# Kernel optimization log

Hardware: AMD Instinct MI355X
Metric: run time of the kernel (lower is better)

Reference implementation:

```python
import jax, jax.numpy as jnp
import numpy as np

L, T, DIN, DOUT = 64, 8192, 128, 128

def setup_inputs() -> dict:
    key = jax.random.key(0)
    k1, k2, k3 = jax.random.split(key, 3)
    x = jax.random.normal(k1, (L, T, DIN), dtype=jnp.float32)
    w = jax.random.normal(k2, (L, DIN, DOUT), dtype=jnp.float32)
    b = jax.random.normal(k3, (L, 1, DOUT), dtype=jnp.float32)
    return {"x": x, "w": w, "b": b}

def reference(x, w, b):
    # grouped GEMM: per-layer matmul x[l] @ w[l], fused bias add
    out = jnp.einsum('lti,lio->lto', x, w) + b  # [L, T, DOUT]
    return out
```

## Files before the change

### kernel.cpp

```cpp
#include <hip/hip_runtime.h>
#include <hip/hip_bf16.h>

#define L_N 64
#define T_N 8192
#define K_N 128
#define N_N 128
#define BM  128

typedef __attribute__((ext_vector_type(8))) short short8;
typedef __attribute__((ext_vector_type(4))) float f32x4;

__device__ __forceinline__ unsigned short f2bf(float f) {
    union { float f; unsigned u; } c; c.f = f;
    return (unsigned short)((c.u + 0x7fffu + ((c.u >> 16) & 1u)) >> 16);
}

__global__ __launch_bounds__(256) void wT_kernel(const float* __restrict__ w,
                                                 unsigned short* __restrict__ wT) {
    __shared__ float lds[128 * 129];
    const int l = blockIdx.x;
    const float* wl = w + (size_t)l * (K_N * N_N);
    const int tid = threadIdx.x;
    #pragma unroll 4
    for (int i = 0; i < 64; ++i) {
        int idx = i * 256 + tid;
        int k = idx >> 7, n = idx & 127;
        lds[k * 129 + n] = wl[idx];
    }
    __syncthreads();
    unsigned short* o = wT + (size_t)l * (K_N * N_N);
    #pragma unroll 4
    for (int i = 0; i < 64; ++i) {
        int idx = i * 256 + tid;
        int n = idx >> 7, k = idx & 127;
        o[idx] = f2bf(lds[k * 129 + n]);
    }
}

__global__ __launch_bounds__(256) void gl_kernel(const float* __restrict__ x,
                                                 const unsigned short* __restrict__ wT,
                                                 const float* __restrict__ bias,
                                                 float* __restrict__ out) {
    __shared__ unsigned short xs [BM  * K_N];
    __shared__ unsigned short wsh[N_N * K_N];

    const int tid = threadIdx.x;
    const int l  = blockIdx.x >> 6;
    const int t0 = (blockIdx.x & 63) * BM;
    const float* xg = x + ((size_t)l * T_N + t0) * K_N;

    #pragma unroll
    for (int i = 0; i < 16; ++i) {
        int f = i * 256 + tid;
        const float4 v = ((const float4*)xg)[f];
        int row = f >> 5;
        int kc  = (f & 31) * 4;
        union { unsigned short s[4]; unsigned long long u; } p;
        p.s[0] = f2bf(v.x); p.s[1] = f2bf(v.y); p.s[2] = f2bf(v.z); p.s[3] = f2bf(v.w);
        int us = (row * K_N + kc) ^ ((row & 7) << 3);
        *(unsigned long long*)&xs[us] = p.u;
    }
    const unsigned short* wg = wT + (size_t)l * (K_N * N_N);
    #pragma unroll
    for (int i = 0; i < 8; ++i) {
        int c = i * 256 + tid;
        short8 v = ((const short8*)wg)[c];
        int row = c >> 4;
        int us = (c * 8) ^ ((row & 7) << 3);
        *(short8*)&wsh[us] = v;
    }
    __syncthreads();

    const int wid  = tid >> 6;
    const int lane = tid & 63;
    const int wm = wid >> 1, wn = wid & 1;
    const int lr = lane & 15;
    const int lg = lane >> 4;

    f32x4 acc[4][4];
    #pragma unroll
    for (int mi = 0; mi < 4; ++mi)
        #pragma unroll
        for (int ni = 0; ni < 4; ++ni)
            acc[mi][ni] = (f32x4){0.f, 0.f, 0.f, 0.f};

    #pragma unroll
    for (int kk = 0; kk < 4; ++kk) {
        const int kbase = kk * 32 + lg * 8;
        short8 a[4], bq[4];
        #pragma unroll
        for (int mi = 0; mi < 4; ++mi) {
            int row = wm * 64 + mi * 16 + lr;
            a[mi] = *(const short8*)&xs[(row * K_N + kbase) ^ ((row & 7) << 3)];
        }
        #pragma unroll
        for (int ni = 0; ni < 4; ++ni) {
            int row = wn * 64 + ni * 16 + lr;
            bq[ni] = *(const short8*)&wsh[(row * K_N + kbase) ^ ((row & 7) << 3)];
        }
        #pragma unroll
        for (int mi = 0; mi < 4; ++mi)
            #pragma unroll
            for (int ni = 0; ni < 4; ++ni)
                acc[mi][ni] = __builtin_amdgcn_mfma_f32_16x16x32_bf16(
                                  a[mi], bq[ni], acc[mi][ni], 0, 0, 0);
    }

    float bv[4];
    #pragma unroll
    for (int ni = 0; ni < 4; ++ni)
        bv[ni] = bias[l * N_N + wn * 64 + ni * 16 + lr];

    float* og = out + ((size_t)l * T_N + t0) * N_N;
    #pragma unroll
    for (int mi = 0; mi < 4; ++mi) {
        #pragma unroll
        for (int ni = 0; ni < 4; ++ni) {
            const int col   = wn * 64 + ni * 16 + lr;
            const int rbase = wm * 64 + mi * 16 + lg * 4;
            #pragma unroll
            for (int j = 0; j < 4; ++j)
                og[(size_t)(rbase + j) * N_N + col] = acc[mi][ni][j] + bv[ni];
        }
    }
}

extern "C" void kernel_launch(void* const* d_in, const int* in_sizes, int n_in,
                              void* d_out, int out_size, void* d_ws, size_t ws_size,
                              hipStream_t stream) {
    const float* x = (const float*)d_in[0];
    const float* w = (const float*)d_in[1];
    const float* b = (const float*)d_in[2];
    float* out = (float*)d_out;
    unsigned short* wT = (unsigned short*)d_ws;

    wT_kernel<<<L_N, 256, 0, stream>>>(w, wT);
    gl_kernel<<<L_N * (T_N / BM), 256, 0, stream>>>(x, wT, b, out);
}
```

Baseline: 116.6 us.

## Drop LDS staging; load MFMA fragments directly from global with pre-fragmented weights

The weight prep kernel now writes bf16 weights already laid out in MFMA fragment order, so each lane loads its B operand straight from global memory. The GEMM kernel drops shared memory and __syncthreads entirely: each wave owns a 32-row strip, loads x fragments directly from global, converts them to bf16 in registers, and swaps the operand roles so accumulators map to contiguous output columns, which allows float4 stores. It also adds an XCD-aware block index swizzle and a launch-bounds occupancy hint. The aim is to remove LDS round-trips and barriers and to vectorize stores, at the cost of redundant weight reads across waves and less coalesced x loads.

Result: slower. 142.2 us (+21.9%).

```diff
diff --git a/kernel.cpp b/kernel.cpp
--- a/kernel.cpp
+++ b/kernel.cpp
@@ -5,7 +5,6 @@
 #define T_N 8192
 #define K_N 128
 #define N_N 128
-#define BM  128
 
 typedef __attribute__((ext_vector_type(8))) short short8;
 typedef __attribute__((ext_vector_type(4))) float f32x4;
@@ -15,112 +14,107 @@
     return (unsigned short)((c.u + 0x7fffu + ((c.u >> 16) & 1u)) >> 16);
 }
 
-__global__ __launch_bounds__(256) void wT_kernel(const float* __restrict__ w,
-                                                 unsigned short* __restrict__ wT) {
-    __shared__ float lds[128 * 129];
+__global__ __launch_bounds__(256) void wfrag_kernel(const float* __restrict__ w,
+                                                    unsigned short* __restrict__ wf) {
+    __shared__ float lds[K_N * 129];
     const int l = blockIdx.x;
     const float* wl = w + (size_t)l * (K_N * N_N);
     const int tid = threadIdx.x;
-    #pragma unroll 4
-    for (int i = 0; i < 64; ++i) {
-        int idx = i * 256 + tid;
-        int k = idx >> 7, n = idx & 127;
-        lds[k * 129 + n] = wl[idx];
+    #pragma unroll
+    for (int i = 0; i < 16; ++i) {
+        int f = i * 256 + tid;
+        float4 v = ((const float4*)wl)[f];
+        int k = f >> 5, n = (f & 31) * 4;
+        lds[k * 129 + n + 0] = v.x;
+        lds[k * 129 + n + 1] = v.y;
+        lds[k * 129 + n + 2] = v.z;
+        lds[k * 129 + n + 3] = v.w;
     }
     __syncthreads();
-    unsigned short* o = wT + (size_t)l * (K_N * N_N);
-    #pragma unroll 4
-    for (int i = 0; i < 64; ++i) {
-        int idx = i * 256 + tid;
-        int n = idx >> 7, k = idx & 127;
-        o[idx] = f2bf(lds[k * 129 + n]);
+    unsigned short* o = wf + (size_t)l * (N_N * K_N);
+    #pragma unroll
+    for (int c = 0; c < 16; ++c) {
+        int chunk = c * 256 + tid;
+        int j0   = (chunk & 1) * 4;
+        int lane = (chunk >> 1) & 63;
+        int kk   = (chunk >> 7) & 3;
+        int ni   = chunk >> 9;
+        int n  = ni * 16 + (lane & 15);
+        int kb = kk * 32 + (lane >> 4) * 8 + j0;
+        ushort4 ov;
+        ov.x = f2bf(lds[(kb + 0) * 129 + n]);
+        ov.y = f2bf(lds[(kb + 1) * 129 + n]);
+        ov.z = f2bf(lds[(kb + 2) * 129 + n]);
+        ov.w = f2bf(lds[(kb + 3) * 129 + n]);
+        ((ushort4*)o)[chunk] = ov;
     }
 }
 
-__global__ __launch_bounds__(256) void gl_kernel(const float* __restrict__ x,
-                                                 const unsigned short* __restrict__ wT,
-                                                 const float* __restrict__ bias,
-                                                 float* __restrict__ out) {
-    __shared__ unsigned short xs [BM  * K_N];
-    __shared__ unsigned short wsh[N_N * K_N];
+__global__ __launch_bounds__(256, 3) void gl_kernel(const float* __restrict__ x,
+                                                    const unsigned short* __restrict__ wf,
+                                                    const float* __restrict__ bias,
+                                                    float* __restrict__ out) {
+    const int tid  = threadIdx.x;
+    const int lane = tid & 63;
+    const int wid  = tid >> 6;
+    const int lr   = lane & 15;
+    const int lg   = lane >> 4;
 
-    const int tid = threadIdx.x;
-    const int l  = blockIdx.x >> 6;
-    const int t0 = (blockIdx.x & 63) * BM;
-    const float* xg = x + ((size_t)l * T_N + t0) * K_N;
+    const int bid = blockIdx.x;
+    const int swz = (bid & 7) * 512 + (bid >> 3);
+    const int l    = swz >> 6;
+    const int tile = swz & 63;
+    const int strip = tile * 128 + wid * 32;
 
+    const float* xg = x + ((size_t)l * T_N + strip) * K_N;
+    const unsigned short* wl = wf + (size_t)l * (N_N * K_N);
+
+    f32x4 acc[2][8];
     #pragma unroll
-    for (int i = 0; i < 16; ++i) {
-        int f = i * 256 + tid;
-        const float4 v = ((const float4*)xg)[f];
-        int row = f >> 5;
-        int kc  = (f & 31) * 4;
-        union { unsigned short s[4]; unsigned long long u; } p;
-        p.s[0] = f2bf(v.x); p.s[1] = f2bf(v.y); p.s[2] = f2bf(v.z); p.s[3] = f2bf(v.w);
-        int us = (row * K_N + kc) ^ ((row & 7) << 3);
-        *(unsigned long long*)&xs[us] = p.u;
-    }
-    const unsigned short* wg = wT + (size_t)l * (K_N * N_N);
-    #pragma unroll
-    for (int i = 0; i < 8; ++i) {
-        int c = i * 256 + tid;
-        short8 v = ((const short8*)wg)[c];
-        int row = c >> 4;
-        int us = (c * 8) ^ ((row & 7) << 3);
-        *(short8*)&wsh[us] = v;
-    }
-    __syncthreads();
-
-    const int wid  = tid >> 6;
-    const int lane = tid & 63;
-    const int wm = wid >> 1, wn = wid & 1;
-    const int lr = lane & 15;
-    const int lg = lane >> 4;
-
-    f32x4 acc[4][4];
-    #pragma unroll
-    for (int mi = 0; mi < 4; ++mi)
+    for (int mi = 0; mi < 2; ++mi)
         #pragma unroll
-        for (int ni = 0; ni < 4; ++ni)
+        for (int ni = 0; ni < 8; ++ni)
             acc[mi][ni] = (f32x4){0.f, 0.f, 0.f, 0.f};
 
     #pragma unroll
     for (int kk = 0; kk < 4; ++kk) {
-        const int kbase = kk * 32 + lg * 8;
-        short8 a[4], bq[4];
+        short8 xb[2];
         #pragma unroll
-        for (int mi = 0; mi < 4; ++mi) {
-            int row = wm * 64 + mi * 16 + lr;
-            a[mi] = *(const short8*)&xs[(row * K_N + kbase) ^ ((row & 7) << 3)];
+        for (int mi = 0; mi < 2; ++mi) {
+            const float* p = xg + (size_t)(mi * 16 + lr) * K_N + kk * 32 + lg * 8;
+            const float4 u0 = *(const float4*)p;
+            const float4 u1 = *(const float4*)(p + 4);
+            union { unsigned short s[8]; short8 v; } pk;
+            pk.s[0] = f2bf(u0.x); pk.s[1] = f2bf(u0.y);
+            pk.s[2] = f2bf(u0.z); pk.s[3] = f2bf(u0.w);
+            pk.s[4] = f2bf(u1.x); pk.s[5] = f2bf(u1.y);
+            pk.s[6] = f2bf(u1.z); pk.s[7] = f2bf(u1.w);
+            xb[mi] = pk.v;
         }
+        short8 wv[8];
         #pragma unroll
-        for (int ni = 0; ni < 4; ++ni) {
-            int row = wn * 64 + ni * 16 + lr;
-            bq[ni] = *(const short8*)&wsh[(row * K_N + kbase) ^ ((row & 7) << 3)];
+        for (int ni = 0; ni < 8; ++ni)
+            wv[ni] = *(const short8*)(wl + ((size_t)(ni * 4 + kk) * 64 + lane) * 8);
+        #pragma unroll
+        for (int ni = 0; ni < 8; ++ni) {
+            acc[0][ni] = __builtin_amdgcn_mfma_f32_16x16x32_bf16(wv[ni], xb[0], acc[0][ni], 0, 0, 0);
+            acc[1][ni] = __builtin_amdgcn_mfma_f32_16x16x32_bf16(wv[ni], xb[1], acc[1][ni], 0, 0, 0);
         }
-        #pragma unroll
-        for (int mi = 0; mi < 4; ++mi)
-            #pragma unroll
-            for (int ni = 0; ni < 4; ++ni)
-                acc[mi][ni] = __builtin_amdgcn_mfma_f32_16x16x32_bf16(
-                                  a[mi], bq[ni], acc[mi][ni], 0, 0, 0);
     }
 
-    float bv[4];
+    const float* bl = bias + l * N_N;
+    float* og = out + ((size_t)l * T_N + strip) * N_N;
     #pragma unroll
-    for (int ni = 0; ni < 4; ++ni)
-        bv[ni] = bias[l * N_N + wn * 64 + ni * 16 + lr];
-
-    float* og = out + ((size_t)l * T_N + t0) * N_N;
-    #pragma unroll
-    for (int mi = 0; mi < 4; ++mi) {
+    for (int ni = 0; ni < 8; ++ni) {
+        const float4 bv = *(const float4*)(bl + ni * 16 + lg * 4);
         #pragma unroll
-        for (int ni = 0; ni < 4; ++ni) {
-            const int col   = wn * 64 + ni * 16 + lr;
-            const int rbase = wm * 64 + mi * 16 + lg * 4;
-            #pragma unroll
-            for (int j = 0; j < 4; ++j)
-                og[(size_t)(rbase + j) * N_N + col] = acc[mi][ni][j] + bv[ni];
+        for (int mi = 0; mi < 2; ++mi) {
+            float4 r;
+            r.x = acc[mi][ni][0] + bv.x;
+            r.y = acc[mi][ni][1] + bv.y;
+            r.z = acc[mi][ni][2] + bv.z;
+            r.w = acc[mi][ni][3] + bv.w;
+            *(float4*)(og + (size_t)(mi * 16 + lr) * N_N + ni * 16 + lg * 4) = r;
         }
     }
 }
@@ -132,8 +126,8 @@
     const float* w = (const float*)d_in[1];
     const float* b = (const float*)d_in[2];
     float* out = (float*)d_out;
-    unsigned short* wT = (unsigned short*)d_ws;
+    unsigned short* wf = (unsigned short*)d_ws;
 
-    wT_kernel<<<L_N, 256, 0, stream>>>(w, wT);
-    gl_kernel<<<L_N * (T_N / BM), 256, 0, stream>>>(x, wT, b, out);
+    wfrag_kernel<<<L_N, 256, 0, stream>>>(w, wf);
+    gl_kernel<<<L_N * (T_N / 128), 256, 0, stream>>>(x, wf, b, out);
 }
```
